# Kernel tuning notes

Measured on AMD Instinct MI355X. Metric: run time of the kernel, lower is better.

The kernel has to match this reference:

```python
import jax, jax.numpy as jnp
import numpy as np

N = 100000          # nodes
E = 1600000         # edges
DIMS = [128, 64, 64, 47]  # in_feats -> hidden -> hidden -> n_classes
EPS = 1e-5


def setup_inputs() -> dict:
    key = jax.random.key(0)
    ks = jax.random.split(key, 10)
    d = {
        "features": jax.random.normal(ks[0], (N, DIMS[0]), jnp.float32),
        "src": jax.random.randint(ks[1], (E,), 0, N, dtype=jnp.int64),
        "dst": jax.random.randint(ks[2], (E,), 0, N, dtype=jnp.int64),
    }
    # GraphConv weights (glorot-ish) + bias
    for i in range(3):
        fan_in, fan_out = DIMS[i], DIMS[i + 1]
        scale = jnp.sqrt(2.0 / (fan_in + fan_out)).astype(jnp.float32)
        d[f"W{i}"] = jax.random.normal(ks[3 + i], (fan_in, fan_out), jnp.float32) * scale
        d[f"b{i}"] = jnp.zeros((fan_out,), jnp.float32)
    # BatchNorm affine params for the first two layers
    for i in range(2):
        d[f"gamma{i}"] = jnp.ones((DIMS[i + 1],), jnp.float32)
        d[f"beta{i}"] = jnp.zeros((DIMS[i + 1],), jnp.float32)
    return d


def _degree_isqrt(idx):
    # clamp degree to >=1 like DGL, then D^{-1/2}
    deg = jax.ops.segment_sum(jnp.ones((E,), jnp.float32), idx, num_segments=N)
    return jax.lax.rsqrt(jnp.maximum(deg, 1.0))


def _graph_conv(h, W, b, src, dst, out_isqrt, in_isqrt):
    # DGL GraphConv, norm='both': h' = D_in^{-1/2} A D_out^{-1/2} h W + b
    h = h * out_isqrt[:, None]
    if W.shape[0] > W.shape[1]:  # mult W first when it shrinks features (DGL order)
        h = h @ W
        h = jax.ops.segment_sum(h[src], dst, num_segments=N)
    else:
        h = jax.ops.segment_sum(h[src], dst, num_segments=N)
        h = h @ W
    return h * in_isqrt[:, None] + b


def _batch_norm(h, gamma, beta):
    mu = h.mean(axis=0)
    var = h.var(axis=0)  # biased, as torch BatchNorm uses for normalization
    return gamma * (h - mu) * jax.lax.rsqrt(var + EPS) + beta


def reference(features, src, dst, W0, b0, W1, b1, W2, b2,
              gamma0, beta0, gamma1, beta1):
    out_isqrt = _degree_isqrt(src)
    in_isqrt = _degree_isqrt(dst)
    Ws = [(W0, b0), (W1, b1), (W2, b2)]
    bns = [(gamma0, beta0), (gamma1, beta1)]
    h = features
    for i, (W, b) in enumerate(Ws):
        # dropout (p=0.5) before last layer only -> identity in eval mode
        h = _graph_conv(h, W, b, src, dst, out_isqrt, in_isqrt)
        if i < len(Ws) - 1:
            h = _batch_norm(h, *bns[i])
            h = jax.nn.relu(h)
    return h
```

## Files before the change

### kernel.cpp

```cpp
#include <hip/hip_runtime.h>
#include <hip/hip_bf16.h>
#include <hip/hip_fp16.h>

#define BN_EPS 1e-5f
#define N_MAX 100000
#define CAP 64
#define NB_MAX 391
#define BCAP 8192

typedef __attribute__((ext_vector_type(8))) _Float16 half8;
typedef __attribute__((ext_vector_type(4))) float floatx4;

__device__ __attribute__((aligned(16))) float g_wsf[130 * N_MAX + 16384];
__device__ int   g_wsi[(2 + CAP) * N_MAX + NB_MAX * BCAP + NB_MAX + 64];

__device__ void wt_fill(const float* __restrict__ W, __half* __restrict__ Wt,
                        int KIN, int KOUT, int ROWS) {
    for (int i = threadIdx.x; i < ROWS * KIN; i += 256) {
        const int c = i / KIN, k = i - c * KIN;
        Wt[c * KIN + k] = (c < KOUT) ? __float2half_rn(W[k * KOUT + c]) : __float2half_rn(0.0f);
    }
}
__global__ __launch_bounds__(256)
void k_setup(const float* __restrict__ W0, const float* __restrict__ W1,
             const float* __restrict__ W2, __half* __restrict__ Wt0,
             __half* __restrict__ Wt1, __half* __restrict__ Wt2,
             int* __restrict__ degs, int* __restrict__ gcur,
             float* __restrict__ stats, int n, int nb) {
    const int b = blockIdx.x;
    if (b == 0)      wt_fill(W0, Wt0, 128, 64, 64);
    else if (b == 1) wt_fill(W1, Wt1, 64, 64, 64);
    else if (b == 2) wt_fill(W2, Wt2, 64, 47, 48);
    else {
        for (int i = (b - 3) * 256 + threadIdx.x; i < n; i += (gridDim.x - 3) * 256)
            degs[i] = 0;
        if (b == 3) {
            for (int i = threadIdx.x; i < nb; i += 256) gcur[i] = 0;
            stats[threadIdx.x] = 0.0f;
        }
    }
}

__global__ __launch_bounds__(256)
void k_bin(const int* __restrict__ src, const int* __restrict__ dst,
           int* __restrict__ gcur, int* __restrict__ degs,
           int* __restrict__ pairs, int E, int nb) {
    __shared__ int dh[NB_MAX], db[NB_MAX], dc[NB_MAX];
    const int tid = threadIdx.x;
    for (int i = tid; i < nb; i += 256) { dh[i] = 0; dc[i] = 0; }
    __syncthreads();
    const int e0 = blockIdx.x * 4096;
    int ss[16], dd[16];
#pragma unroll
    for (int i = 0; i < 16; ++i) {
        int e = e0 + i * 256 + tid;
        if (e < E) {
            ss[i] = src[e]; dd[i] = dst[e];
            atomicAdd(&dh[dd[i] >> 8], 1);
            atomicAdd(&degs[ss[i]], 1);
        } else ss[i] = -1;
    }
    __syncthreads();
    for (int i = tid; i < nb; i += 256) db[i] = atomicAdd(&gcur[i], dh[i]);
    __syncthreads();
#pragma unroll
    for (int i = 0; i < 16; ++i) {
        if (ss[i] >= 0) {
            int b = dd[i] >> 8;
            int idx = db[b] + atomicAdd(&dc[b], 1);
            if (idx < BCAP) pairs[b * BCAP + idx] = (ss[i] << 8) | (dd[i] & 255);
        }
    }
}

__global__ __launch_bounds__(256)
void k_slab(const int* __restrict__ gcur, const int* __restrict__ pairs,
            const int* __restrict__ degs, int* __restrict__ slab,
            int* __restrict__ cnt, float* __restrict__ isq_d,
            float* __restrict__ isq_s, int n) {
    __shared__ int c[256];
    const int tid = threadIdx.x;
    const int d0 = blockIdx.x * 256;
    c[tid] = 0;
    __syncthreads();
    const int m = min(gcur[blockIdx.x], BCAP);
    const int base = blockIdx.x * BCAP;
    for (int i = tid; i < m; i += 256) {
        int p = pairs[base + i];
        int dl = p & 255;
        int slot = atomicAdd(&c[dl], 1);
        if (slot < CAP) slab[(size_t)(d0 + dl) * CAP + slot] = p >> 8;
    }
    __syncthreads();
    int d = d0 + tid;
    if (d < n) {
        cnt[d] = c[tid];
        isq_d[d] = rsqrtf(fmaxf((float)c[tid], 1.0f));
        isq_s[d] = rsqrtf(fmaxf((float)degs[d], 1.0f));
    }
}

template<bool SB, bool FBN>
__global__ __launch_bounds__(256)
void k_agg(const int* __restrict__ cnt, const int* __restrict__ slab,
           const __half* __restrict__ in, const float* __restrict__ isq_d,
           const float* __restrict__ bias, const float* __restrict__ stats,
           const float* __restrict__ gamma, const float* __restrict__ beta,
           const float* __restrict__ isq_s, __half* __restrict__ out, int n) {
    const int d = (int)((blockIdx.x * 256u + threadIdx.x) >> 6);
    if (d >= n) return;
    const int lane = threadIdx.x & 63;
    const int sub = lane >> 3;
    const int fc = (lane & 7) << 3;

    float bsc[8], bsh[8];
    if (FBN) {
        const float invn = 1.0f / (float)n;
#pragma unroll
        for (int k = 0; k < 8; ++k) {
            const int f = fc + k;
            const float mu = stats[f] * invn;
            const float var = stats[64 + f] * invn - mu * mu;
            const float s = gamma[f] * rsqrtf(var + BN_EPS);
            bsc[k] = s;
            bsh[k] = beta[f] - mu * s;
        }
    }

    const int m = min(cnt[d], CAP);
    const int* cs = slab + (size_t)d * CAP;
    float a[8] = {};
    for (int e = 0; e < m; e += 16) {
#pragma unroll
        for (int u = 0; u < 2; ++u) {
            int j = e + u * 8 + sub;
            if (j < m) {
                int s = cs[j];
                float iss;
                if (FBN) iss = isq_s[s];
                const uint4 v = *(const uint4*)(in + (size_t)s * 64 + fc);
                const float2 f0 = __half22float2(*(const __half2*)&v.x);
                const float2 f1 = __half22float2(*(const __half2*)&v.y);
                const float2 f2 = __half22float2(*(const __half2*)&v.z);
                const float2 f3 = __half22float2(*(const __half2*)&v.w);
                float h[8] = {f0.x, f0.y, f1.x, f1.y, f2.x, f2.y, f3.x, f3.y};
                if (FBN) {
#pragma unroll
                    for (int k = 0; k < 8; ++k)
                        h[k] = fmaxf(fmaf(h[k], bsc[k], bsh[k]), 0.0f) * iss;
                }
#pragma unroll
                for (int k = 0; k < 8; ++k) a[k] += h[k];
            }
        }
    }
#pragma unroll
    for (int sh = 8; sh <= 32; sh <<= 1) {
#pragma unroll
        for (int k = 0; k < 8; ++k) a[k] += __shfl_xor(a[k], sh);
    }
    if (sub == 0) {
        if (SB) {
            const float sd = isq_d[d];
            const float4 b0 = *(const float4*)(bias + fc);
            const float4 b1 = *(const float4*)(bias + fc + 4);
            a[0] = a[0] * sd + b0.x; a[1] = a[1] * sd + b0.y;
            a[2] = a[2] * sd + b0.z; a[3] = a[3] * sd + b0.w;
            a[4] = a[4] * sd + b1.x; a[5] = a[5] * sd + b1.y;
            a[6] = a[6] * sd + b1.z; a[7] = a[7] * sd + b1.w;
        }
        __half2 h01 = __floats2half2_rn(a[0], a[1]);
        __half2 h23 = __floats2half2_rn(a[2], a[3]);
        __half2 h45 = __floats2half2_rn(a[4], a[5]);
        __half2 h67 = __floats2half2_rn(a[6], a[7]);
        uint4 u;
        u.x = *(const unsigned*)&h01; u.y = *(const unsigned*)&h23;
        u.z = *(const unsigned*)&h45; u.w = *(const unsigned*)&h67;
        *(uint4*)(out + (size_t)d * 64 + fc) = u;
    }
}

template<int KIN, int KOUTR, bool HIN, bool HOUT, bool BIAS>
__global__ __launch_bounds__(256)
void k_gemm_mfma(const void* __restrict__ Xv, const float* __restrict__ rowscale,
                 const __half* __restrict__ Wt, const float* __restrict__ bias,
                 void* __restrict__ Cv, int n) {
    constexpr int NK = KIN / 32;
    constexpr int NT = (KOUTR + 15) / 16;
    constexpr int CHUNKS = KIN / 8;
    __shared__ __align__(16) unsigned short Xs[64 * KIN];
    const int tid = threadIdx.x;
    const int row0 = blockIdx.x * 64;

#pragma unroll
    for (int it = 0; it < (64 * CHUNKS) / 256; ++it) {
        const int idx = it * 256 + tid;
        const int row = idx / CHUNKS;
        const int ch = idx & (CHUNKS - 1);
        const int rg = row0 + row;
        uint4 v = {0u, 0u, 0u, 0u};
        if (rg < n) {
            if (HIN) {
                v = *(const uint4*)((const __half*)Xv + (size_t)rg * KIN + ch * 8);
            } else {
                const float* Xf = (const float*)Xv;
                const float4 f0 = *(const float4*)(Xf + (size_t)rg * KIN + ch * 8);
                const float4 f1 = *(const float4*)(Xf + (size_t)rg * KIN + ch * 8 + 4);
                __half2 h01 = __floats2half2_rn(f0.x, f0.y);
                __half2 h23 = __floats2half2_rn(f0.z, f0.w);
                __half2 h45 = __floats2half2_rn(f1.x, f1.y);
                __half2 h67 = __floats2half2_rn(f1.z, f1.w);
                v.x = *(const unsigned*)&h01; v.y = *(const unsigned*)&h23;
                v.z = *(const unsigned*)&h45; v.w = *(const unsigned*)&h67;
            }
        }
        const int sch = ch ^ (row & 7);
        *(uint4*)(&Xs[row * KIN + sch * 8]) = v;
    }

    const int lane = tid & 63;
    const int lc = lane & 15;
    const int lg = lane >> 4;
    half8 bf[NK][NT];
#pragma unroll
    for (int s = 0; s < NK; ++s)
#pragma unroll
        for (int t = 0; t < NT; ++t)
            bf[s][t] = *(const half8*)(Wt + (size_t)(t * 16 + lc) * KIN + s * 32 + lg * 8);

    __syncthreads();

    const int w = tid >> 6;
    const int rowl = 16 * w + lc;
    floatx4 acc[NT];
#pragma unroll
    for (int t = 0; t < NT; ++t) acc[t] = 0.0f;
#pragma unroll
    for (int s = 0; s < NK; ++s) {
        const int ch = s * 4 + lg;
        const int sch = ch ^ (rowl & 7);
        const half8 a = *(const half8*)(&Xs[rowl * KIN + sch * 8]);
#pragma unroll
        for (int t = 0; t < NT; ++t)
            acc[t] = __builtin_amdgcn_mfma_f32_16x16x32_f16(a, bf[s][t], acc[t], 0, 0, 0);
    }

    const int rbase = row0 + 16 * w + lg * 4;
#pragma unroll
    for (int t = 0; t < NT; ++t) {
        const int c = t * 16 + lc;
#pragma unroll
        for (int r = 0; r < 4; ++r) {
            const int rg = rbase + r;
            if (rg >= n) continue;
            float v = acc[t][r] * rowscale[rg];
            if (BIAS) v += bias[c];
            if (HOUT) {
                ((__half*)Cv)[(size_t)rg * KOUTR + c] = __float2half_rn(v);
            } else {
                if (KOUTR == 64 || c < KOUTR)
                    ((float*)Cv)[(size_t)rg * KOUTR + c] = v;
            }
        }
    }
}

template<bool HIN>
__global__ __launch_bounds__(256)
void k_bn_stats(const void* __restrict__ Av, float* __restrict__ stats, int n) {
    const int f = threadIdx.x & 63;
    const int sub = threadIdx.x >> 6;
    float s = 0.0f, q = 0.0f;
    for (int i = blockIdx.x * 4 + sub; i < n; i += gridDim.x * 4) {
        float h;
        if (HIN) h = __half2float(((const __half*)Av)[(size_t)i * 64 + f]);
        else     h = ((const float*)Av)[(size_t)i * 64 + f];
        s += h;
        q += h * h;
    }
    __shared__ float ls[4][64], lq[4][64];
    ls[sub][f] = s; lq[sub][f] = q;
    __syncthreads();
    if (sub == 0) {
        s = ls[0][f] + ls[1][f] + ls[2][f] + ls[3][f];
        q = lq[0][f] + lq[1][f] + lq[2][f] + lq[3][f];
        atomicAdd(&stats[f], s);
        atomicAdd(&stats[64 + f], q);
    }
}

extern "C" void kernel_launch(void* const* d_in, const int* in_sizes, int n_in,
                              void* d_out, int out_size, void* d_ws, size_t ws_size,
                              hipStream_t stream) {
    const float* feat = (const float*)d_in[0];
    const int* src  = (const int*)d_in[1];
    const int* dst  = (const int*)d_in[2];
    const float* W0  = (const float*)d_in[3];
    const float* b0  = (const float*)d_in[4];
    const float* W1  = (const float*)d_in[5];
    const float* b1  = (const float*)d_in[6];
    const float* W2  = (const float*)d_in[7];
    const float* b2  = (const float*)d_in[8];
    const float* g0  = (const float*)d_in[9];
    const float* be0 = (const float*)d_in[10];
    const float* g1  = (const float*)d_in[11];
    const float* be1 = (const float*)d_in[12];

    const int n = out_size / 47;
    const int E = in_sizes[1];
    const int nb = (n + 255) >> 8;

    float* wsf = nullptr; int* wsi = nullptr;
    hipGetSymbolAddress((void**)&wsf, HIP_SYMBOL(g_wsf));
    hipGetSymbolAddress((void**)&wsi, HIP_SYMBOL(g_wsi));
    float* isq_s = wsf;
    float* isq_d = wsf + n;
    float* buf1  = wsf + 2 * (size_t)n;
    float* buf2  = buf1 + (size_t)n * 64;
    float* stats = buf2 + (size_t)n * 64;
    __half* Wt0  = (__half*)(stats + 256);
    __half* Wt1  = Wt0 + 64 * 128;
    __half* Wt2  = Wt1 + 64 * 64;
    __half* buf1h = (__half*)buf1;
    __half* buf2h = (__half*)buf2;
    int* cnt     = wsi;
    int* degs    = wsi + n;
    int* slab    = wsi + 2 * (size_t)n;
    int* pairs   = slab + (size_t)N_MAX * CAP;
    int* gcur    = pairs + (size_t)NB_MAX * BCAP;

    const int gB = (E + 4095) / 4096;
    const int gW = (n + 3) / 4;
    const int gG = (n + 63) / 64;

    k_setup<<<35, 256, 0, stream>>>(W0, W1, W2, Wt0, Wt1, Wt2, degs, gcur, stats, n, nb);
    k_bin<<<gB, 256, 0, stream>>>(src, dst, gcur, degs, pairs, E, nb);
    k_slab<<<nb, 256, 0, stream>>>(gcur, pairs, degs, slab, cnt, isq_d, isq_s, n);

    k_gemm_mfma<128, 64, false, true, false><<<gG, 256, 0, stream>>>(feat, isq_s, Wt0, nullptr, buf1h, n);
    k_agg<true, false><<<gW, 256, 0, stream>>>(cnt, slab, buf1h, isq_d, b0,
                                               nullptr, nullptr, nullptr, nullptr, buf2h, n);
    k_bn_stats<true><<<512, 256, 0, stream>>>(buf2h, stats, n);

    k_agg<false, true><<<gW, 256, 0, stream>>>(cnt, slab, buf2h, nullptr, nullptr,
                                               stats, g0, be0, isq_s, buf1h, n);
    k_gemm_mfma<64, 64, true, true, true><<<gG, 256, 0, stream>>>(buf1h, isq_d, Wt1, b1, buf2h, n);
    k_bn_stats<true><<<512, 256, 0, stream>>>(buf2h, stats + 128, n);

    k_agg<false, true><<<gW, 256, 0, stream>>>(cnt, slab, buf2h, nullptr, nullptr,
                                               stats + 128, g1, be1, isq_s, buf1h, n);
    k_gemm_mfma<64, 47, true, false, true><<<gG, 256, 0, stream>>>(buf1h, isq_d, Wt2, b2, (float*)d_out, n);
}
```

Measured before the change: 492.2 us.

## Replace global atomic out-degree counting with binned source bytes counted in shared memory

```diff
diff --git a/kernel.cpp b/kernel.cpp
--- a/kernel.cpp
+++ b/kernel.cpp
@@ -12,7 +12,8 @@
 typedef __attribute__((ext_vector_type(4))) float floatx4;
 
 __device__ __attribute__((aligned(16))) float g_wsf[130 * N_MAX + 16384];
-__device__ int   g_wsi[(2 + CAP) * N_MAX + NB_MAX * BCAP + NB_MAX + 64];
+__device__ int   g_wsi[(1 + CAP) * N_MAX + NB_MAX * BCAP + 2 * NB_MAX + 64];
+__device__ unsigned char g_wsb[NB_MAX * BCAP];
 
 __device__ void wt_fill(const float* __restrict__ W, __half* __restrict__ Wt,
                         int KIN, int KOUT, int ROWS) {
@@ -25,29 +26,27 @@
 void k_setup(const float* __restrict__ W0, const float* __restrict__ W1,
              const float* __restrict__ W2, __half* __restrict__ Wt0,
              __half* __restrict__ Wt1, __half* __restrict__ Wt2,
-             int* __restrict__ degs, int* __restrict__ gcur,
-             float* __restrict__ stats, int n, int nb) {
+             int* __restrict__ gcur, int* __restrict__ scur,
+             float* __restrict__ stats, int nb) {
     const int b = blockIdx.x;
     if (b == 0)      wt_fill(W0, Wt0, 128, 64, 64);
     else if (b == 1) wt_fill(W1, Wt1, 64, 64, 64);
     else if (b == 2) wt_fill(W2, Wt2, 64, 47, 48);
     else {
-        for (int i = (b - 3) * 256 + threadIdx.x; i < n; i += (gridDim.x - 3) * 256)
-            degs[i] = 0;
-        if (b == 3) {
-            for (int i = threadIdx.x; i < nb; i += 256) gcur[i] = 0;
-            stats[threadIdx.x] = 0.0f;
-        }
+        for (int i = threadIdx.x; i < nb; i += 256) { gcur[i] = 0; scur[i] = 0; }
+        stats[threadIdx.x] = 0.0f;
     }
 }
 
 __global__ __launch_bounds__(256)
 void k_bin(const int* __restrict__ src, const int* __restrict__ dst,
-           int* __restrict__ gcur, int* __restrict__ degs,
-           int* __restrict__ pairs, int E, int nb) {
+           int* __restrict__ gcur, int* __restrict__ scur,
+           int* __restrict__ pairs, unsigned char* __restrict__ sbytes,
+           int E, int nb) {
     __shared__ int dh[NB_MAX], db[NB_MAX], dc[NB_MAX];
+    __shared__ int sh[NB_MAX], sb[NB_MAX], sc[NB_MAX];
     const int tid = threadIdx.x;
-    for (int i = tid; i < nb; i += 256) { dh[i] = 0; dc[i] = 0; }
+    for (int i = tid; i < nb; i += 256) { dh[i] = 0; sh[i] = 0; dc[i] = 0; sc[i] = 0; }
     __syncthreads();
     const int e0 = blockIdx.x * 4096;
     int ss[16], dd[16];
@@ -57,11 +56,14 @@
         if (e < E) {
             ss[i] = src[e]; dd[i] = dst[e];
             atomicAdd(&dh[dd[i] >> 8], 1);
-            atomicAdd(&degs[ss[i]], 1);
+            atomicAdd(&sh[ss[i] >> 8], 1);
         } else ss[i] = -1;
     }
     __syncthreads();
-    for (int i = tid; i < nb; i += 256) db[i] = atomicAdd(&gcur[i], dh[i]);
+    for (int i = tid; i < nb; i += 256) {
+        db[i] = atomicAdd(&gcur[i], dh[i]);
+        sb[i] = atomicAdd(&scur[i], sh[i]);
+    }
     __syncthreads();
 #pragma unroll
     for (int i = 0; i < 16; ++i) {
@@ -69,34 +71,47 @@
             int b = dd[i] >> 8;
             int idx = db[b] + atomicAdd(&dc[b], 1);
             if (idx < BCAP) pairs[b * BCAP + idx] = (ss[i] << 8) | (dd[i] & 255);
-        }
-    }
-}
-
-__global__ __launch_bounds__(256)
-void k_slab(const int* __restrict__ gcur, const int* __restrict__ pairs,
-            const int* __restrict__ degs, int* __restrict__ slab,
-            int* __restrict__ cnt, float* __restrict__ isq_d,
-            float* __restrict__ isq_s, int n) {
+            int b2 = ss[i] >> 8;
+            int i2 = sb[b2] + atomicAdd(&sc[b2], 1);
+            if (i2 < BCAP) sbytes[b2 * BCAP + i2] = (unsigned char)(ss[i] & 255);
+        }
+    }
+}
+
+__global__ __launch_bounds__(256)
+void k_csr(const int* __restrict__ gcur, const int* __restrict__ scur,
+           const int* __restrict__ pairs, const unsigned char* __restrict__ sbytes,
+           int* __restrict__ slab, int* __restrict__ cnt,
+           float* __restrict__ isq_d, float* __restrict__ isq_s, int n, int nb) {
     __shared__ int c[256];
     const int tid = threadIdx.x;
-    const int d0 = blockIdx.x * 256;
     c[tid] = 0;
     __syncthreads();
-    const int m = min(gcur[blockIdx.x], BCAP);
-    const int base = blockIdx.x * BCAP;
-    for (int i = tid; i < m; i += 256) {
-        int p = pairs[base + i];
-        int dl = p & 255;
-        int slot = atomicAdd(&c[dl], 1);
-        if (slot < CAP) slab[(size_t)(d0 + dl) * CAP + slot] = p >> 8;
-    }
-    __syncthreads();
-    int d = d0 + tid;
-    if (d < n) {
-        cnt[d] = c[tid];
-        isq_d[d] = rsqrtf(fmaxf((float)c[tid], 1.0f));
-        isq_s[d] = rsqrtf(fmaxf((float)degs[d], 1.0f));
+    if (blockIdx.x < (unsigned)nb) {
+        const int bb = blockIdx.x;
+        const int d0 = bb * 256;
+        const int m = min(gcur[bb], BCAP);
+        const int base = bb * BCAP;
+        for (int i = tid; i < m; i += 256) {
+            int p = pairs[base + i];
+            int dl = p & 255;
+            int slot = atomicAdd(&c[dl], 1);
+            if (slot < CAP) slab[(size_t)(d0 + dl) * CAP + slot] = p >> 8;
+        }
+        __syncthreads();
+        int d = d0 + tid;
+        if (d < n) {
+            cnt[d] = c[tid];
+            isq_d[d] = rsqrtf(fmaxf((float)c[tid], 1.0f));
+        }
+    } else {
+        const int bb = blockIdx.x - nb;
+        const int m = min(scur[bb], BCAP);
+        const int base = bb * BCAP;
+        for (int i = tid; i < m; i += 256) atomicAdd(&c[sbytes[base + i]], 1);
+        __syncthreads();
+        int s = bb * 256 + tid;
+        if (s < n) isq_s[s] = rsqrtf(fmaxf((float)c[tid], 1.0f));
     }
 }
 
@@ -310,9 +325,10 @@
     const int E = in_sizes[1];
     const int nb = (n + 255) >> 8;
 
-    float* wsf = nullptr; int* wsi = nullptr;
+    float* wsf = nullptr; int* wsi = nullptr; unsigned char* wsb = nullptr;
     hipGetSymbolAddress((void**)&wsf, HIP_SYMBOL(g_wsf));
     hipGetSymbolAddress((void**)&wsi, HIP_SYMBOL(g_wsi));
+    hipGetSymbolAddress((void**)&wsb, HIP_SYMBOL(g_wsb));
     float* isq_s = wsf;
     float* isq_d = wsf + n;
     float* buf1  = wsf + 2 * (size_t)n;
@@ -324,18 +340,18 @@
     __half* buf1h = (__half*)buf1;
     __half* buf2h = (__half*)buf2;
     int* cnt     = wsi;
-    int* degs    = wsi + n;
-    int* slab    = wsi + 2 * (size_t)n;
-    int* pairs   = slab + (size_t)N_MAX * CAP;
+    int* slab    = wsi + n;
+    int* pairs   = wsi + (size_t)(1 + CAP) * n;
     int* gcur    = pairs + (size_t)NB_MAX * BCAP;
+    int* scur    = gcur + NB_MAX;
 
     const int gB = (E + 4095) / 4096;
     const int gW = (n + 3) / 4;
     const int gG = (n + 63) / 64;
 
-    k_setup<<<35, 256, 0, stream>>>(W0, W1, W2, Wt0, Wt1, Wt2, degs, gcur, stats, n, nb);
-    k_bin<<<gB, 256, 0, stream>>>(src, dst, gcur, degs, pairs, E, nb);
-    k_slab<<<nb, 256, 0, stream>>>(gcur, pairs, degs, slab, cnt, isq_d, isq_s, n);
+    k_setup<<<4, 256, 0, stream>>>(W0, W1, W2, Wt0, Wt1, Wt2, gcur, scur, stats, nb);
+    k_bin<<<gB, 256, 0, stream>>>(src, dst, gcur, scur, pairs, wsb, E, nb);
+    k_csr<<<2 * nb, 256, 0, stream>>>(gcur, scur, pairs, wsb, slab, cnt, isq_d, isq_s, n, nb);
 
     k_gemm_mfma<128, 64, false, true, false><<<gG, 256, 0, stream>>>(feat, isq_s, Wt0, nullptr, buf1h, n);
     k_agg<true, false><<<gW, 256, 0, stream>>>(cnt, slab, buf1h, isq_d, b0,
```

Measured after the change: 452.9 us. -8.0%, faster.
